# Optimization experiments

Hardware: AMD Instinct MI355X
Metric: run time of the kernel (lower is better)

Reference implementation:

```python
import jax, jax.numpy as jnp
import numpy as np

B, S, H = 2, 2048, 2048
NH = 16
HD = H // NH  # 128


def setup_inputs() -> dict:
    key = jax.random.key(0)
    ks = jax.random.split(key, 10)
    std = 0.02
    hidden_states = jax.random.normal(ks[0], (B, S, H), dtype=jnp.float32)
    # causal additive mask, broadcastable to [B, NH, S, S]
    causal = jnp.tril(jnp.ones((S, S), dtype=jnp.float32))
    attention_mask = jnp.where(causal == 1, 0.0, -1e9)[None, None, :, :] * jnp.ones((B, 1, 1, 1), jnp.float32)
    Wq = jax.random.normal(ks[1], (H, H), jnp.float32) * std
    Wk = jax.random.normal(ks[2], (H, H), jnp.float32) * std
    Wv = jax.random.normal(ks[3], (H, H), jnp.float32) * std
    Wo = jax.random.normal(ks[4], (H, H), jnp.float32) * std
    bq = jnp.zeros((H,), jnp.float32)
    bk = jnp.zeros((H,), jnp.float32)
    bv = jnp.zeros((H,), jnp.float32)
    bo = jnp.zeros((H,), jnp.float32)
    return {"hidden_states": hidden_states, "attention_mask": attention_mask,
            "Wq": Wq, "bq": bq, "Wk": Wk, "bk": bk, "Wv": Wv, "bv": bv, "Wo": Wo, "bo": bo}


def reference(hidden_states, attention_mask, Wq, bq, Wk, bk, Wv, bv, Wo, bo):
    b, s, _ = hidden_states.shape
    q = (hidden_states @ Wq + bq).reshape(b, s, NH, HD)
    k = (hidden_states @ Wk + bk).reshape(b, s, NH, HD)
    v = (hidden_states @ Wv + bv).reshape(b, s, NH, HD)
    # [b, h, s_q, s_k]
    scores = jnp.einsum('bqhd,bkhd->bhqk', q, k) / jnp.sqrt(jnp.float32(HD))
    scores = scores + attention_mask
    probs = jax.nn.softmax(scores, axis=-1)
    out = jnp.einsum('bhqk,bkhd->bqhd', probs, v).reshape(b, s, H)
    return out @ Wo + bo
```

## Files before the change

kernel.cpp:

```cpp
#include <hip/hip_runtime.h>
#include <hip/hip_bf16.h>
#include <stdint.h>

#define SEQ 2048
#define HID 2048
#define NHEAD 16
#define HDIM 128

typedef __attribute__((ext_vector_type(8))) short short8;
typedef __attribute__((ext_vector_type(4))) float f32x4;

__device__ __forceinline__ short f2bf(float f) {
  union { float f; unsigned u; } x; x.f = f;
  unsigned r = (x.u + 0x7FFFu + ((x.u >> 16) & 1u)) >> 16;
  return (short)r;
}

__device__ __forceinline__ void async_ld16(const void* g, void* l) {
  __builtin_amdgcn_global_load_lds(
      (__attribute__((address_space(1))) void*)g,
      (__attribute__((address_space(3))) void*)l, 16, 0, 0);
}

__global__ __launch_bounds__(256) void k_convert(const float* __restrict__ X,
                                                 short* __restrict__ Xb) {
  int i = blockIdx.x * 256 + threadIdx.x;
  float4 v = ((const float4*)X)[i];
  short4 o;
  o.x = f2bf(v.x); o.y = f2bf(v.y); o.z = f2bf(v.z); o.w = f2bf(v.w);
  ((short4*)Xb)[i] = o;
}

__global__ __launch_bounds__(256) void k_transpose(const float* __restrict__ W0,
                                                   const float* __restrict__ W1,
                                                   const float* __restrict__ W2,
                                                   const float* __restrict__ W3,
                                                   short* __restrict__ Wt) {
  __shared__ float t[64][65];
  int z = blockIdx.z;
  const float* W = (z == 0) ? W0 : (z == 1) ? W1 : (z == 2) ? W2 : W3;
  short* o = Wt + (size_t)z * HID * HID;
  int k0 = blockIdx.x * 64, n0 = blockIdx.y * 64;
  int tx = threadIdx.x & 63, ty = threadIdx.x >> 6;
#pragma unroll
  for (int i = 0; i < 16; ++i) {
    int r = ty * 16 + i;
    t[r][tx] = W[(size_t)(k0 + r) * HID + n0 + tx];
  }
  __syncthreads();
#pragma unroll
  for (int i = 0; i < 16; ++i) {
    int r = ty * 16 + i;
    o[(size_t)(n0 + r) * HID + k0 + tx] = f2bf(t[tx][r]);
  }
}

__global__ __launch_bounds__(256, 3) void k_gemm_qkv(const short* __restrict__ A,
                                                     const short* __restrict__ Bt,
                                                     const float* __restrict__ bqp,
                                                     const float* __restrict__ bkp,
                                                     const float* __restrict__ bvp,
                                                     short* __restrict__ Qb,
                                                     short* __restrict__ Kb,
                                                     short* __restrict__ VtG) {
  __shared__ short smem[128 * 136];
  short* As = smem;
  short* Bs = smem + 128 * 64;
  const int tid = threadIdx.x;
  const int wave = tid >> 6, lane = tid & 63;
  const int col = lane & 15, quad = lane >> 4;
  const int wm = wave >> 1, wn = wave & 1;
  const int m0 = blockIdx.y * 128;
  const int n0g = blockIdx.x * 128;
  const int j = n0g >> 11;
  const int n0 = n0g & 2047;
  const int K = HID;
  const float* bias = (j == 0) ? bqp : (j == 1) ? bkp : bvp;

  const int rS = (lane >> 3), cS = lane & 7;
  f32x4 acc[4][4];
  for (int i = 0; i < 4; ++i)
    for (int jj = 0; jj < 4; ++jj)
      acc[i][jj] = (f32x4){0.f, 0.f, 0.f, 0.f};

  for (int k0 = 0; k0 < K; k0 += 64) {
    __syncthreads();
    for (int i = 0; i < 4; ++i) {
      int rowb = wave * 8 + i * 32;
      int row = rowb + rS;
      int src = cS ^ (row & 7);
      async_ld16(A + (size_t)(m0 + row) * K + k0 + src * 8,
                 (char*)As + (size_t)rowb * 128);
      async_ld16(Bt + (size_t)(n0g + row) * K + k0 + src * 8,
                 (char*)Bs + (size_t)rowb * 128);
    }
    __syncthreads();
    for (int h = 0; h < 2; ++h) {
      short8 af[4], bf[4];
      for (int mi = 0; mi < 4; ++mi)
        af[mi] = *(const short8*)(As + (wm * 64 + mi * 16 + col) * 64 +
                                  ((h * 4 + quad) ^ (col & 7)) * 8);
      for (int ni = 0; ni < 4; ++ni)
        bf[ni] = *(const short8*)(Bs + (wn * 64 + ni * 16 + col) * 64 +
                                  ((h * 4 + quad) ^ (col & 7)) * 8);
      for (int mi = 0; mi < 4; ++mi)
        for (int ni = 0; ni < 4; ++ni)
          acc[mi][ni] =
              __builtin_amdgcn_mfma_f32_16x16x32_bf16(af[mi], bf[ni], acc[mi][ni], 0, 0, 0);
    }
  }

  __syncthreads();
  short* T = smem;
  if (j == 2) {
    for (int ni = 0; ni < 4; ++ni) {
      int n = wn * 64 + ni * 16 + col;
      float bv = bias[n0 + n];
      for (int mi = 0; mi < 4; ++mi)
        for (int r = 0; r < 4; ++r) {
          int m = wm * 64 + mi * 16 + quad * 4 + r;
          T[n * 136 + m] = f2bf(acc[mi][ni][r] + bv);
        }
    }
    __syncthreads();
    int h = n0 >> 7;
    int b = m0 >> 11, s0l = m0 & 2047;
    int rr = tid >> 1, halfc = tid & 1;
    short* o = VtG + ((size_t)(b * NHEAD + h) * HDIM + rr) * SEQ + s0l;
    for (int i = 0; i < 8; ++i) {
      int chunk = halfc * 8 + i;
      short8 v = *(const short8*)(T + rr * 136 + chunk * 8);
      *(short8*)(o + chunk * 8) = v;
    }
    return;
  }

  for (int ni = 0; ni < 4; ++ni) {
    int n = wn * 64 + ni * 16 + col;
    float bv = bias[n0 + n];
    for (int mi = 0; mi < 4; ++mi)
      for (int r = 0; r < 4; ++r) {
        int m = wm * 64 + mi * 16 + quad * 4 + r;
        T[m * 136 + n] = f2bf(acc[mi][ni][r] + bv);
      }
  }
  __syncthreads();
  short* out = (j == 0) ? Qb : Kb;
  int h = n0 >> 7;
  for (int i = 0; i < 8; ++i) {
    int c = i * 256 + tid;
    int m = c >> 4, ch = c & 15;
    int mm = m0 + m;
    int b = mm >> 11, s = mm & 2047;
    short8 v = *(const short8*)(T + m * 136 + ch * 8);
    *(short8*)(out + ((size_t)(b * NHEAD + h) * SEQ + s) * HDIM + ch * 8) = v;
  }
}

__global__ __launch_bounds__(256, 3) void k_gemm_o(const short* __restrict__ A,
                                                   const short* __restrict__ Bt,
                                                   const float* __restrict__ bias,
                                                   float* __restrict__ out) {
  __shared__ short As[128 * 64];
  __shared__ short Bs[128 * 64];
  const int tid = threadIdx.x;
  const int wave = tid >> 6, lane = tid & 63;
  const int col = lane & 15, quad = lane >> 4;
  const int wm = wave >> 1, wn = wave & 1;
  const int m0 = blockIdx.y * 128, n0 = blockIdx.x * 128;
  const int K = HID;
  const int rS = (lane >> 3), cS = lane & 7;

  f32x4 acc[4][4];
  for (int i = 0; i < 4; ++i)
    for (int jj = 0; jj < 4; ++jj)
      acc[i][jj] = (f32x4){0.f, 0.f, 0.f, 0.f};

  for (int k0 = 0; k0 < K; k0 += 64) {
    __syncthreads();
    for (int i = 0; i < 4; ++i) {
      int rowb = wave * 8 + i * 32;
      int row = rowb + rS;
      int src = cS ^ (row & 7);
      async_ld16(A + (size_t)(m0 + row) * K + k0 + src * 8,
                 (char*)As + (size_t)rowb * 128);
      async_ld16(Bt + (size_t)(n0 + row) * K + k0 + src * 8,
                 (char*)Bs + (size_t)rowb * 128);
    }
    __syncthreads();
    for (int h = 0; h < 2; ++h) {
      short8 af[4], bf[4];
      for (int mi = 0; mi < 4; ++mi)
        af[mi] = *(const short8*)(As + (wm * 64 + mi * 16 + col) * 64 +
                                  ((h * 4 + quad) ^ (col & 7)) * 8);
      for (int ni = 0; ni < 4; ++ni)
        bf[ni] = *(const short8*)(Bs + (wn * 64 + ni * 16 + col) * 64 +
                                  ((h * 4 + quad) ^ (col & 7)) * 8);
      for (int mi = 0; mi < 4; ++mi)
        for (int ni = 0; ni < 4; ++ni)
          acc[mi][ni] =
              __builtin_amdgcn_mfma_f32_16x16x32_bf16(af[mi], bf[ni], acc[mi][ni], 0, 0, 0);
    }
  }

  for (int ni = 0; ni < 4; ++ni) {
    int n = n0 + wn * 64 + ni * 16 + col;
    float bv = bias[n];
    for (int mi = 0; mi < 4; ++mi)
      for (int r = 0; r < 4; ++r) {
        int m = m0 + wm * 64 + mi * 16 + quad * 4 + r;
        out[(size_t)m * HID + n] = acc[mi][ni][r] + bv;
      }
  }
}

__global__ __launch_bounds__(1024) void k_attn(const short* __restrict__ Qb,
                                               const short* __restrict__ Kb,
                                               const short* __restrict__ VtG,
                                               short* __restrict__ AO) {
  __shared__ short Ks[2][64 * 128];
  __shared__ short Vt[2][128 * 64];
  __shared__ short Pb[16 * 16 * 72];

  const int bx = blockIdx.x;
  const int p = bx & 7;
  const int h = (bx >> 3) & 15;
  const int b = bx >> 7;
  const int tid = threadIdx.x;
  const int wave = tid >> 6, lane = tid & 63;
  const int col = lane & 15, quad = lane >> 4;

  const bool hiw = wave < 8;
  const int wslot = wave & 7;
  const int qb = hiw ? (15 - p) : p;
  const int q0 = qb * 128 + wslot * 16;
  const int nt_w = 2 * qb + 2;
  const int nt = 2 * (15 - p) + 2;

  const size_t ho = (size_t)(b * NHEAD + h) * SEQ * HDIM;
  const short* Qh = Qb + ho;
  const short* Kh = Kb + ho;
  const short* Vh = VtG + ho;

  const float scale = 0.08838834764831845f;
  short8 ones;
  for (int i = 0; i < 8; ++i) ones[i] = (short)0x3F80;

  const int rowK = tid >> 4, c16 = tid & 15;
  const int srcK = c16 ^ (rowK & 7);
  const int rowV = tid >> 3, c8 = tid & 7;
  const int srcV = c8 ^ (rowV & 7);
  short* Pw = Pb + wave * 16 * 72;

  short8 qf[4];
  for (int f = 0; f < 4; ++f)
    qf[f] = *(const short8*)(Qh + (size_t)(q0 + col) * HDIM + f * 32 + quad * 8);

  f32x4 o[8], osum;
  for (int t = 0; t < 8; ++t) o[t] = (f32x4){0.f, 0.f, 0.f, 0.f};
  osum = (f32x4){0.f, 0.f, 0.f, 0.f};

  async_ld16(Kh + (size_t)rowK * HDIM + srcK * 8, (char*)Ks[0] + tid * 16);
  async_ld16(Vh + (size_t)rowV * SEQ + srcV * 8, (char*)Vt[0] + tid * 16);

  for (int kb = 0; kb < nt; ++kb) {
    __syncthreads();
    const int cur = kb & 1;
    if (kb + 1 < nt) {
      async_ld16(Kh + (size_t)((kb + 1) * 64 + rowK) * HDIM + srcK * 8,
                 (char*)Ks[cur ^ 1] + tid * 16);
      async_ld16(Vh + (size_t)rowV * SEQ + (kb + 1) * 64 + srcV * 8,
                 (char*)Vt[cur ^ 1] + tid * 16);
    }
    if (kb >= nt_w) continue;

    const short* KsC = Ks[cur];
    const short* VtC = Vt[cur];

    f32x4 s[4];
    for (int nf = 0; nf < 4; ++nf) s[nf] = (f32x4){0.f, 0.f, 0.f, 0.f};
    for (int f = 0; f < 4; ++f)
      for (int nf = 0; nf < 4; ++nf) {
        short8 kf = *(const short8*)(KsC + (nf * 16 + col) * 128 +
                                     (((f * 4 + quad) ^ (col & 7)) * 8));
        s[nf] = __builtin_amdgcn_mfma_f32_16x16x32_bf16(qf[f], kf, s[nf], 0, 0, 0);
      }

    const bool diag = (kb >= 2 * qb);
    for (int nf = 0; nf < 4; ++nf)
      for (int r = 0; r < 4; ++r) {
        float e = __expf(s[nf][r] * scale - 8.0f);
        if (diag) {
          int key = kb * 64 + nf * 16 + col;
          int q = q0 + quad * 4 + r;
          if (key > q) e = 0.f;
        }
        Pw[(quad * 4 + r) * 72 + nf * 16 + col] = f2bf(e);
      }

    for (int kk = 0; kk < 2; ++kk) {
      short8 pa = *(const short8*)(Pw + col * 72 + kk * 32 + quad * 8);
      osum = __builtin_amdgcn_mfma_f32_16x16x32_bf16(pa, ones, osum, 0, 0, 0);
      for (int t = 0; t < 8; ++t) {
        short8 vf = *(const short8*)(VtC + (t * 16 + col) * 64 +
                                     (((kk * 4 + quad) ^ (col & 7)) * 8));
        o[t] = __builtin_amdgcn_mfma_f32_16x16x32_bf16(pa, vf, o[t], 0, 0, 0);
      }
    }
  }

  for (int r = 0; r < 4; ++r) {
    float inv = 1.f / osum[r];
    int q = q0 + quad * 4 + r;
    for (int t = 0; t < 8; ++t)
      AO[((size_t)(b * SEQ + q)) * HID + h * HDIM + 16 * t + col] = f2bf(o[t][r] * inv);
  }
}

extern "C" void kernel_launch(void* const* d_in, const int* in_sizes, int n_in,
                              void* d_out, int out_size, void* d_ws, size_t ws_size,
                              hipStream_t stream) {
  const float* X  = (const float*)d_in[0];
  const float* Wq = (const float*)d_in[2];
  const float* bq = (const float*)d_in[3];
  const float* Wk = (const float*)d_in[4];
  const float* bk = (const float*)d_in[5];
  const float* Wv = (const float*)d_in[6];
  const float* bv = (const float*)d_in[7];
  const float* Wo = (const float*)d_in[8];
  const float* bo = (const float*)d_in[9];

  char* ws = (char*)d_ws;
  short* Xb  = (short*)(ws);
  short* Wt  = (short*)(ws + (16ull << 20));
  short* Qb  = (short*)(ws + (48ull << 20));
  short* Kb  = (short*)(ws + (64ull << 20));
  short* VtG = (short*)(ws + (80ull << 20));
  short* AO  = (short*)(ws + (96ull << 20));

  short* Wto = Wt + (size_t)3 * HID * HID;

  k_convert<<<8192, 256, 0, stream>>>(X, Xb);
  k_transpose<<<dim3(32, 32, 4), 256, 0, stream>>>(Wq, Wk, Wv, Wo, Wt);

  k_gemm_qkv<<<dim3(48, 32), 256, 0, stream>>>(Xb, Wt, bq, bk, bv, Qb, Kb, VtG);

  k_attn<<<2 * NHEAD * 8, 1024, 0, stream>>>(Qb, Kb, VtG, AO);

  k_gemm_o<<<dim3(16, 32), 256, 0, stream>>>(AO, Wto, bo, (float*)d_out);
}
```

Measured before the change: 384.8 us.

## Merge prep kernels, load K directly from global in attention, remap block order

Fuses the X conversion and the weight transpose into a single launch, removing one kernel launch. The attention kernel no longer stages K tiles in LDS; each wave reads its K fragments straight from global memory (through cache), which cuts LDS usage and async copies but gives up the shared reuse of K across the 16 waves. The block index mapping is also changed so that heads and batches vary fastest and the causal work level varies slowest, which changes scheduling order and L2 locality.

```diff
diff --git a/kernel.cpp b/kernel.cpp
--- a/kernel.cpp
+++ b/kernel.cpp
@@ -22,26 +22,29 @@
       (__attribute__((address_space(3))) void*)l, 16, 0, 0);
 }
 
-__global__ __launch_bounds__(256) void k_convert(const float* __restrict__ X,
-                                                 short* __restrict__ Xb) {
-  int i = blockIdx.x * 256 + threadIdx.x;
-  float4 v = ((const float4*)X)[i];
-  short4 o;
-  o.x = f2bf(v.x); o.y = f2bf(v.y); o.z = f2bf(v.z); o.w = f2bf(v.w);
-  ((short4*)Xb)[i] = o;
-}
-
-__global__ __launch_bounds__(256) void k_transpose(const float* __restrict__ W0,
-                                                   const float* __restrict__ W1,
-                                                   const float* __restrict__ W2,
-                                                   const float* __restrict__ W3,
-                                                   short* __restrict__ Wt) {
+__global__ __launch_bounds__(256) void k_prep(const float* __restrict__ X,
+                                              short* __restrict__ Xb,
+                                              const float* __restrict__ W0,
+                                              const float* __restrict__ W1,
+                                              const float* __restrict__ W2,
+                                              const float* __restrict__ W3,
+                                              short* __restrict__ Wt) {
   __shared__ float t[64][65];
-  int z = blockIdx.z;
+  const int bid = blockIdx.x, tid = threadIdx.x;
+  if (bid < 8192) {
+    int i = bid * 256 + tid;
+    float4 v = ((const float4*)X)[i];
+    short4 o;
+    o.x = f2bf(v.x); o.y = f2bf(v.y); o.z = f2bf(v.z); o.w = f2bf(v.w);
+    ((short4*)Xb)[i] = o;
+    return;
+  }
+  int idx = bid - 8192;
+  int z = idx >> 10, rem = idx & 1023;
+  int k0 = (rem & 31) * 64, n0 = (rem >> 5) * 64;
   const float* W = (z == 0) ? W0 : (z == 1) ? W1 : (z == 2) ? W2 : W3;
   short* o = Wt + (size_t)z * HID * HID;
-  int k0 = blockIdx.x * 64, n0 = blockIdx.y * 64;
-  int tx = threadIdx.x & 63, ty = threadIdx.x >> 6;
+  int tx = tid & 63, ty = tid >> 6;
 #pragma unroll
   for (int i = 0; i < 16; ++i) {
     int r = ty * 16 + i;
@@ -218,14 +221,13 @@
                                                const short* __restrict__ Kb,
                                                const short* __restrict__ VtG,
                                                short* __restrict__ AO) {
-  __shared__ short Ks[2][64 * 128];
   __shared__ short Vt[2][128 * 64];
   __shared__ short Pb[16 * 16 * 72];
 
   const int bx = blockIdx.x;
-  const int p = bx & 7;
-  const int h = (bx >> 3) & 15;
-  const int b = bx >> 7;
+  const int p = bx >> 5;
+  const int h = bx & 15;
+  const int b = (bx >> 4) & 1;
   const int tid = threadIdx.x;
   const int wave = tid >> 6, lane = tid & 63;
   const int col = lane & 15, quad = lane >> 4;
@@ -246,8 +248,6 @@
   short8 ones;
   for (int i = 0; i < 8; ++i) ones[i] = (short)0x3F80;
 
-  const int rowK = tid >> 4, c16 = tid & 15;
-  const int srcK = c16 ^ (rowK & 7);
   const int rowV = tid >> 3, c8 = tid & 7;
   const int srcV = c8 ^ (rowV & 7);
   short* Pw = Pb + wave * 16 * 72;
@@ -260,29 +260,26 @@
   for (int t = 0; t < 8; ++t) o[t] = (f32x4){0.f, 0.f, 0.f, 0.f};
   osum = (f32x4){0.f, 0.f, 0.f, 0.f};
 
-  async_ld16(Kh + (size_t)rowK * HDIM + srcK * 8, (char*)Ks[0] + tid * 16);
   async_ld16(Vh + (size_t)rowV * SEQ + srcV * 8, (char*)Vt[0] + tid * 16);
 
   for (int kb = 0; kb < nt; ++kb) {
     __syncthreads();
     const int cur = kb & 1;
     if (kb + 1 < nt) {
-      async_ld16(Kh + (size_t)((kb + 1) * 64 + rowK) * HDIM + srcK * 8,
-                 (char*)Ks[cur ^ 1] + tid * 16);
       async_ld16(Vh + (size_t)rowV * SEQ + (kb + 1) * 64 + srcV * 8,
                  (char*)Vt[cur ^ 1] + tid * 16);
     }
     if (kb >= nt_w) continue;
 
-    const short* KsC = Ks[cur];
     const short* VtC = Vt[cur];
+    const short* Kt = Kh + (size_t)(kb * 64) * HDIM;
 
     f32x4 s[4];
     for (int nf = 0; nf < 4; ++nf) s[nf] = (f32x4){0.f, 0.f, 0.f, 0.f};
     for (int f = 0; f < 4; ++f)
       for (int nf = 0; nf < 4; ++nf) {
-        short8 kf = *(const short8*)(KsC + (nf * 16 + col) * 128 +
-                                     (((f * 4 + quad) ^ (col & 7)) * 8));
+        short8 kf = *(const short8*)(Kt + (size_t)(nf * 16 + col) * HDIM +
+                                     f * 32 + quad * 8);
         s[nf] = __builtin_amdgcn_mfma_f32_16x16x32_bf16(qf[f], kf, s[nf], 0, 0, 0);
       }
 
@@ -340,8 +337,7 @@
 
   short* Wto = Wt + (size_t)3 * HID * HID;
 
-  k_convert<<<8192, 256, 0, stream>>>(X, Xb);
-  k_transpose<<<dim3(32, 32, 4), 256, 0, stream>>>(Wq, Wk, Wv, Wo, Wt);
+  k_prep<<<8192 + 4096, 256, 0, stream>>>(X, Xb, Wq, Wk, Wv, Wo, Wt);
 
   k_gemm_qkv<<<dim3(48, 32), 256, 0, stream>>>(Xb, Wt, bq, bk, bv, Qb, Kb, VtG);
 
```

Result: slower. 479.4 us (+24.6%).
